# Kernel tuning notes

Measured on AMD Instinct MI355X. Metric: run time of the kernel, lower is better.

The kernel has to match this reference:

```python
import jax, jax.numpy as jnp
import numpy as np

C, H, W = 128, 128, 128
N_LINES = 8192
N_POINTS = 32
POOL = 4
DIM_FC = 1024


def setup_inputs() -> dict:
    key = jax.random.key(0)
    ks = jax.random.split(key, 8)
    feats = jax.random.normal(ks[0], (C, H, W), dtype=jnp.float32)
    # line endpoints (x1,y1,x2,y2) in feature-map pixel coords
    lines = jax.random.uniform(ks[1], (N_LINES, 4), dtype=jnp.float32) * (H - 1)
    d_in = C * (N_POINTS // POOL)  # 1024
    W1 = jax.random.normal(ks[2], (DIM_FC, d_in), dtype=jnp.float32) * 0.02
    b1 = jax.random.normal(ks[3], (DIM_FC,), dtype=jnp.float32) * 0.02
    W2 = jax.random.normal(ks[4], (DIM_FC, DIM_FC), dtype=jnp.float32) * 0.02
    b2 = jax.random.normal(ks[5], (DIM_FC,), dtype=jnp.float32) * 0.02
    W3 = jax.random.normal(ks[6], (4, DIM_FC), dtype=jnp.float32) * 0.02
    b3 = jax.random.normal(ks[7], (4,), dtype=jnp.float32) * 0.02
    return {
        "features_per_image": feats,
        "lines_per_im": lines,
        "W1": W1, "b1": b1, "W2": W2, "b2": b2, "W3": W3, "b3": b3,
        "n_points": N_POINTS,
        "pool_stride": POOL,
    }


def _extract_pt_feats(features, lines, n_points):
    # features: [C, H, W]; lines: [N, 4]
    c, h, w = features.shape
    tspan = jnp.linspace(0.0, 1.0, n_points).astype(features.dtype)  # [P]
    U, V = lines[:, :2], lines[:, 2:]
    # [N, 2, P] -> interpolate endpoints, shift by 0.5 (torch pixel-center convention)
    pts = U[:, :, None] * tspan + V[:, :, None] * (1.0 - tspan) - 0.5
    pts = pts.transpose(0, 2, 1).reshape(-1, 2)  # [N*P, 2]
    px, py = pts[:, 0], pts[:, 1]
    # NOTE: faithful to torch source: px indexes the h-axis but is clamped with w-1,
    # py indexes the w-axis but is clamped with h-1 (harmless here since H == W).
    px0 = jnp.clip(jnp.floor(px), 0.0, w - 1)
    py0 = jnp.clip(jnp.floor(py), 0.0, h - 1)
    px1 = jnp.clip(px0 + 1.0, 0.0, w - 1)
    py1 = jnp.clip(py0 + 1.0, 0.0, h - 1)
    px0i, py0i = px0.astype(jnp.int32), py0.astype(jnp.int32)
    px1i, py1i = px1.astype(jnp.int32), py1.astype(jnp.int32)
    # four irregular gathers + bilinear weights, fused expression. each term: [C, N*P]
    xp = (features[:, px0i, py0i] * ((py1 - py) * (px1 - px))
          + features[:, px0i, py1i] * ((py - py0) * (px1 - px))
          + features[:, px1i, py0i] * ((py1 - py) * (px - px0))
          + features[:, px1i, py1i] * ((py - py0) * (px - px0)))
    return xp.reshape(c, -1, n_points).transpose(1, 0, 2)  # [N, C, P]


def reference(features_per_image, lines_per_im, W1, b1, W2, b2, W3, b3,
              n_points, pool_stride):
    xp = _extract_pt_feats(features_per_image, lines_per_im, n_points)  # [N, C, P]
    n, c, p = xp.shape
    # MaxPool1d(kernel=stride=pool_stride)
    pooled = xp.reshape(n, c, p // pool_stride, pool_stride).max(axis=-1)
    flat = pooled.reshape(n, -1)  # [N, C*(P//s)]
    h1 = jax.nn.relu(flat @ W1.T + b1)
    h2 = jax.nn.relu(h1 @ W2.T + b2)
    return h2 @ W3.T + b3  # [N, 4]
```

## Files before the change

### kernel.cpp

```cpp
#include <hip/hip_runtime.h>
#include <hip/hip_bf16.h>
#include <cstdint>

typedef __attribute__((ext_vector_type(4))) float f32x4;
typedef __attribute__((ext_vector_type(8))) short short8;

#define DEVI __device__ __forceinline__

DEVI uint16_t f2bf(float v) {
    union { float f; uint32_t u; } c; c.f = v;
    uint32_t u = c.u + 0x7FFFu + ((c.u >> 16) & 1u);
    return (uint16_t)(u >> 16);
}
DEVI float bflo(uint32_t u) { union { uint32_t u; float f; } c; c.u = u << 16; return c.f; }
DEVI float bfhi(uint32_t u) { union { uint32_t u; float f; } c; c.u = u & 0xFFFF0000u; return c.f; }

DEVI void async16(const uint16_t* g, uint16_t* l) {
    __builtin_amdgcn_global_load_lds((const __attribute__((address_space(1))) void*)g,
                                     (__attribute__((address_space(3))) void*)l, 16, 0, 0);
}

__global__ __launch_bounds__(256) void prep_feat(const float* __restrict__ f,
                                                 uint16_t* __restrict__ featT) {
    __shared__ uint16_t s[128 * 130];
    const int x = blockIdx.x;
    const float* fx = f + x * 128;
    for (int i = threadIdx.x; i < 16384; i += 256) {
        int c = i >> 7, y = i & 127;
        s[y * 130 + c] = f2bf(fx[c * 16384 + y]);
    }
    __syncthreads();
    uint16_t* o = featT + x * 16384;
    for (int i = threadIdx.x; i < 16384; i += 256) {
        int y = i >> 7, c = i & 127;
        o[i] = s[y * 130 + c];
    }
}

__global__ __launch_bounds__(256) void cvt_w(const float* __restrict__ W1, uint16_t* __restrict__ W1b,
                                             const float* __restrict__ W2, uint16_t* __restrict__ W2b) {
    int i = blockIdx.x * 256 + threadIdx.x;
    float4 a = ((const float4*)W1)[i];
    float4 b = ((const float4*)W2)[i];
    ushort4 pa = { f2bf(a.x), f2bf(a.y), f2bf(a.z), f2bf(a.w) };
    ushort4 pb = { f2bf(b.x), f2bf(b.y), f2bf(b.z), f2bf(b.w) };
    ((ushort4*)W1b)[i] = pa;
    ((ushort4*)W2b)[i] = pb;
}

__global__ __launch_bounds__(256) void extract_k(const float4* __restrict__ lines,
                                                 const uint16_t* __restrict__ featT,
                                                 uint16_t* __restrict__ flat) {
    const int n = blockIdx.x;
    const int tid = threadIdx.x;
    const int lane = tid & 63, wave = tid >> 6;
    const float4 ln = lines[n];
    __shared__ uint16_t ps[1024];
    const uint16_t* fb = featT + lane * 2;

    for (int g2 = 0; g2 < 2; ++g2) {
        const int g = wave * 2 + g2;
        float m0 = -1e30f, m1 = -1e30f;
#pragma unroll
        for (int pp = 0; pp < 4; ++pp) {
            const float t = (float)(g * 4 + pp) * (1.0f / 31.0f);
            const float x = ln.x * t + ln.z * (1.0f - t) - 0.5f;
            const float y = ln.y * t + ln.w * (1.0f - t) - 0.5f;
            const float x0f = fminf(fmaxf(floorf(x), 0.0f), 127.0f);
            const float y0f = fminf(fmaxf(floorf(y), 0.0f), 127.0f);
            const float x1f = fminf(x0f + 1.0f, 127.0f);
            const float y1f = fminf(y0f + 1.0f, 127.0f);
            const int x0 = (int)x0f, x1 = (int)x1f, y0 = (int)y0f, y1 = (int)y1f;
            const float wx1 = x - x0f, wx0 = x1f - x;
            const float wy1 = y - y0f, wy0 = y1f - y;
            const uint32_t u00 = *(const uint32_t*)(fb + ((x0 * 128 + y0) << 7));
            const uint32_t u01 = *(const uint32_t*)(fb + ((x0 * 128 + y1) << 7));
            const uint32_t u10 = *(const uint32_t*)(fb + ((x1 * 128 + y0) << 7));
            const uint32_t u11 = *(const uint32_t*)(fb + ((x1 * 128 + y1) << 7));
            const float w00 = wy0 * wx0, w01 = wy1 * wx0, w10 = wy0 * wx1, w11 = wy1 * wx1;
            const float a = bflo(u00) * w00 + bflo(u01) * w01 + bflo(u10) * w10 + bflo(u11) * w11;
            const float b = bfhi(u00) * w00 + bfhi(u01) * w01 + bfhi(u10) * w10 + bfhi(u11) * w11;
            m0 = fmaxf(m0, a);
            m1 = fmaxf(m1, b);
        }
        ps[lane * 16 + g]     = f2bf(m0);
        ps[lane * 16 + 8 + g] = f2bf(m1);
    }
    __syncthreads();
    *(uint2*)(flat + (size_t)n * 1024 + tid * 4) = ((const uint2*)ps)[tid];
}

template <int RELU>
__global__ __launch_bounds__(256) void gemm_bt(const uint16_t* __restrict__ A,
                                               const uint16_t* __restrict__ B,
                                               const float* __restrict__ bias,
                                               uint16_t* __restrict__ Co,
                                               int M, int N, int K) {
    __shared__ uint16_t As[128 * 32];
    __shared__ uint16_t Bs[128 * 32];
    const int tid = threadIdx.x;
    const int lane = tid & 63, wave = tid >> 6;
    const int nbm = M >> 7;
    const int bm = blockIdx.x % nbm;
    const int bn = blockIdx.x / nbm;
    const int wr = wave >> 1, wc = wave & 1;
    const int l15 = lane & 15, l16 = lane >> 4;

    f32x4 acc[4][4] = {};

    const uint16_t* Ag = A + (size_t)(bm * 128) * K;
    const uint16_t* Bg = B + (size_t)(bn * 128) * K;

    for (int kt = 0; kt < K; kt += 32) {
        if (kt) __syncthreads();
#pragma unroll
        for (int i = 0; i < 2; ++i) {
            const int c = i * 256 + tid;
            const int row = c >> 2, off = (c & 3) * 8;
            async16(Ag + (size_t)row * K + kt + off, &As[c * 8]);
            async16(Bg + (size_t)row * K + kt + off, &Bs[c * 8]);
        }
        __syncthreads();
        short8 a[4], b[4];
#pragma unroll
        for (int fm = 0; fm < 4; ++fm)
            a[fm] = *(const short8*)&As[(wr * 64 + fm * 16 + l15) * 32 + l16 * 8];
#pragma unroll
        for (int fn = 0; fn < 4; ++fn)
            b[fn] = *(const short8*)&Bs[(wc * 64 + fn * 16 + l15) * 32 + l16 * 8];
#pragma unroll
        for (int fm = 0; fm < 4; ++fm)
#pragma unroll
            for (int fn = 0; fn < 4; ++fn)
                acc[fm][fn] = __builtin_amdgcn_mfma_f32_16x16x32_bf16(a[fm], b[fn], acc[fm][fn], 0, 0, 0);
    }

#pragma unroll
    for (int fm = 0; fm < 4; ++fm) {
        const int row = bm * 128 + wr * 64 + fm * 16 + l16 * 4;
#pragma unroll
        for (int fn = 0; fn < 4; ++fn) {
            const int col = bn * 128 + wc * 64 + fn * 16 + l15;
            const float bv = bias[col];
#pragma unroll
            for (int r = 0; r < 4; ++r) {
                float v = acc[fm][fn][r] + bv;
                if (RELU) v = fmaxf(v, 0.0f);
                Co[(size_t)(row + r) * N + col] = f2bf(v);
            }
        }
    }
}

__global__ __launch_bounds__(256) void gemm3_k(const uint16_t* __restrict__ h2,
                                               const float* __restrict__ W3,
                                               const float* __restrict__ b3,
                                               float* __restrict__ out) {
    const int wave = threadIdx.x >> 6, lane = threadIdx.x & 63;
    const int m = blockIdx.x * 4 + wave;
    const uint4* hr = (const uint4*)(h2 + (size_t)m * 1024 + lane * 16);
    const uint4 u0 = hr[0], u1 = hr[1];
    float h[16];
    h[0] = bflo(u0.x); h[1] = bfhi(u0.x); h[2] = bflo(u0.y); h[3] = bfhi(u0.y);
    h[4] = bflo(u0.z); h[5] = bfhi(u0.z); h[6] = bflo(u0.w); h[7] = bfhi(u0.w);
    h[8]  = bflo(u1.x); h[9]  = bfhi(u1.x); h[10] = bflo(u1.y); h[11] = bfhi(u1.y);
    h[12] = bflo(u1.z); h[13] = bfhi(u1.z); h[14] = bflo(u1.w); h[15] = bfhi(u1.w);
    float acc[4];
#pragma unroll
    for (int j = 0; j < 4; ++j) {
        const float4* wr = (const float4*)(W3 + j * 1024 + lane * 16);
        const float4 w0 = wr[0], w1 = wr[1], w2 = wr[2], w3 = wr[3];
        float s;
        s  = h[0] * w0.x;  s += h[1] * w0.y;  s += h[2] * w0.z;  s += h[3] * w0.w;
        s += h[4] * w1.x;  s += h[5] * w1.y;  s += h[6] * w1.z;  s += h[7] * w1.w;
        s += h[8] * w2.x;  s += h[9] * w2.y;  s += h[10] * w2.z; s += h[11] * w2.w;
        s += h[12] * w3.x; s += h[13] * w3.y; s += h[14] * w3.z; s += h[15] * w3.w;
        acc[j] = s;
    }
#pragma unroll
    for (int off = 32; off >= 1; off >>= 1) {
#pragma unroll
        for (int j = 0; j < 4; ++j) acc[j] += __shfl_xor(acc[j], off);
    }
    if (lane == 0) {
        float4 o = { acc[0] + b3[0], acc[1] + b3[1], acc[2] + b3[2], acc[3] + b3[3] };
        *(float4*)(out + (size_t)m * 4) = o;
    }
}

extern "C" void kernel_launch(void* const* d_in, const int* in_sizes, int n_in,
                              void* d_out, int out_size, void* d_ws, size_t ws_size,
                              hipStream_t stream) {
    const float* feats = (const float*)d_in[0];
    const float* lines = (const float*)d_in[1];
    const float* W1 = (const float*)d_in[2];
    const float* b1 = (const float*)d_in[3];
    const float* W2 = (const float*)d_in[4];
    const float* b2 = (const float*)d_in[5];
    const float* W3 = (const float*)d_in[6];
    const float* b3 = (const float*)d_in[7];
    float* out = (float*)d_out;

    char* ws = (char*)d_ws;
    uint16_t* featT = (uint16_t*)(ws);
    uint16_t* W1b   = (uint16_t*)(ws + (4u << 20));
    uint16_t* W2b   = (uint16_t*)(ws + (6u << 20));
    uint16_t* flat  = (uint16_t*)(ws + (8u << 20));
    uint16_t* h1    = (uint16_t*)(ws + (24u << 20));

    prep_feat<<<128, 256, 0, stream>>>(feats, featT);
    cvt_w<<<1024, 256, 0, stream>>>(W1, W1b, W2, W2b);
    extract_k<<<8192, 256, 0, stream>>>((const float4*)lines, featT, flat);
    gemm_bt<1><<<512, 256, 0, stream>>>(flat, W1b, b1, h1, 8192, 1024, 1024);
    gemm_bt<1><<<512, 256, 0, stream>>>(h1, W2b, b2, flat, 8192, 1024, 1024);
    gemm3_k<<<2048, 256, 0, stream>>>(flat, W3, b3, out);
}
```

Before: 98.32 us.

## Fuse final linear layer into second GEMM epilogue and widen K tile with swizzle

The third linear layer (1024->4) is folded into the second GEMM's epilogue. Each block applies ReLU to its tile of h2, multiplies by W3, reduces across lanes with shuffles, and atomically adds partial sums into an output that a new kernel pre-fills with b3. This removes the h2 round trip through memory and one kernel launch. The GEMM K tile grows from 32 to 64 with an XOR-swizzled LDS layout to cut bank conflicts and halve the barrier count, and the feature-transpose and weight-conversion prep kernels are merged into one launch. In exchange, fp32 atomics make the summation order nondeterministic.

```diff
diff --git a/kernel.cpp b/kernel.cpp
--- a/kernel.cpp
+++ b/kernel.cpp
@@ -20,32 +20,38 @@
                                      (__attribute__((address_space(3))) void*)l, 16, 0, 0);
 }
 
-__global__ __launch_bounds__(256) void prep_feat(const float* __restrict__ f,
-                                                 uint16_t* __restrict__ featT) {
-    __shared__ uint16_t s[128 * 130];
-    const int x = blockIdx.x;
-    const float* fx = f + x * 128;
-    for (int i = threadIdx.x; i < 16384; i += 256) {
-        int c = i >> 7, y = i & 127;
-        s[y * 130 + c] = f2bf(fx[c * 16384 + y]);
-    }
-    __syncthreads();
-    uint16_t* o = featT + x * 16384;
-    for (int i = threadIdx.x; i < 16384; i += 256) {
-        int y = i >> 7, c = i & 127;
-        o[i] = s[y * 130 + c];
-    }
-}
-
-__global__ __launch_bounds__(256) void cvt_w(const float* __restrict__ W1, uint16_t* __restrict__ W1b,
-                                             const float* __restrict__ W2, uint16_t* __restrict__ W2b) {
-    int i = blockIdx.x * 256 + threadIdx.x;
-    float4 a = ((const float4*)W1)[i];
-    float4 b = ((const float4*)W2)[i];
-    ushort4 pa = { f2bf(a.x), f2bf(a.y), f2bf(a.z), f2bf(a.w) };
-    ushort4 pb = { f2bf(b.x), f2bf(b.y), f2bf(b.z), f2bf(b.w) };
-    ((ushort4*)W1b)[i] = pa;
-    ((ushort4*)W2b)[i] = pb;
+__global__ __launch_bounds__(256) void init_out(float* __restrict__ out, const float* __restrict__ b3) {
+    const int i = blockIdx.x * 256 + threadIdx.x;
+    float4 b = { b3[0], b3[1], b3[2], b3[3] };
+    ((float4*)out)[i] = b;
+}
+
+__global__ __launch_bounds__(256) void prep_all(const float* __restrict__ f, uint16_t* __restrict__ featT,
+                                                const float* __restrict__ W1, uint16_t* __restrict__ W1b,
+                                                const float* __restrict__ W2, uint16_t* __restrict__ W2b) {
+    if (blockIdx.x < 128) {
+        __shared__ uint16_t s[128 * 130];
+        const int x = blockIdx.x;
+        const float* fx = f + x * 128;
+        for (int i = threadIdx.x; i < 16384; i += 256) {
+            int c = i >> 7, y = i & 127;
+            s[y * 130 + c] = f2bf(fx[c * 16384 + y]);
+        }
+        __syncthreads();
+        uint16_t* o = featT + x * 16384;
+        for (int i = threadIdx.x; i < 16384; i += 256) {
+            int y = i >> 7, c = i & 127;
+            o[i] = s[y * 130 + c];
+        }
+    } else {
+        const int i = (blockIdx.x - 128) * 256 + threadIdx.x;
+        float4 a = ((const float4*)W1)[i];
+        float4 b = ((const float4*)W2)[i];
+        ushort4 pa = { f2bf(a.x), f2bf(a.y), f2bf(a.z), f2bf(a.w) };
+        ushort4 pb = { f2bf(b.x), f2bf(b.y), f2bf(b.z), f2bf(b.w) };
+        ((ushort4*)W1b)[i] = pa;
+        ((ushort4*)W2b)[i] = pb;
+    }
 }
 
 __global__ __launch_bounds__(256) void extract_k(const float4* __restrict__ lines,
@@ -90,14 +96,16 @@
     *(uint2*)(flat + (size_t)n * 1024 + tid * 4) = ((const uint2*)ps)[tid];
 }
 
-template <int RELU>
+template <int FUSE3>
 __global__ __launch_bounds__(256) void gemm_bt(const uint16_t* __restrict__ A,
                                                const uint16_t* __restrict__ B,
                                                const float* __restrict__ bias,
                                                uint16_t* __restrict__ Co,
+                                               const float* __restrict__ W3,
+                                               float* __restrict__ out3,
                                                int M, int N, int K) {
-    __shared__ uint16_t As[128 * 32];
-    __shared__ uint16_t Bs[128 * 32];
+    __shared__ uint16_t As[128 * 64];
+    __shared__ uint16_t Bs[128 * 64];
     const int tid = threadIdx.x;
     const int lane = tid & 63, wave = tid >> 6;
     const int nbm = M >> 7;
@@ -111,80 +119,92 @@
     const uint16_t* Ag = A + (size_t)(bm * 128) * K;
     const uint16_t* Bg = B + (size_t)(bn * 128) * K;
 
-    for (int kt = 0; kt < K; kt += 32) {
+    for (int kt = 0; kt < K; kt += 64) {
         if (kt) __syncthreads();
 #pragma unroll
-        for (int i = 0; i < 2; ++i) {
+        for (int i = 0; i < 4; ++i) {
             const int c = i * 256 + tid;
-            const int row = c >> 2, off = (c & 3) * 8;
-            async16(Ag + (size_t)row * K + kt + off, &As[c * 8]);
-            async16(Bg + (size_t)row * K + kt + off, &Bs[c * 8]);
+            const int row = c >> 3, slot = c & 7;
+            const int s2 = slot ^ (row & 7);
+            async16(Ag + (size_t)row * K + kt + s2 * 8, &As[c * 8]);
+            async16(Bg + (size_t)row * K + kt + s2 * 8, &Bs[c * 8]);
         }
         __syncthreads();
-        short8 a[4], b[4];
-#pragma unroll
-        for (int fm = 0; fm < 4; ++fm)
-            a[fm] = *(const short8*)&As[(wr * 64 + fm * 16 + l15) * 32 + l16 * 8];
-#pragma unroll
-        for (int fn = 0; fn < 4; ++fn)
-            b[fn] = *(const short8*)&Bs[(wc * 64 + fn * 16 + l15) * 32 + l16 * 8];
-#pragma unroll
-        for (int fm = 0; fm < 4; ++fm)
-#pragma unroll
-            for (int fn = 0; fn < 4; ++fn)
-                acc[fm][fn] = __builtin_amdgcn_mfma_f32_16x16x32_bf16(a[fm], b[fn], acc[fm][fn], 0, 0, 0);
-    }
-
-#pragma unroll
-    for (int fm = 0; fm < 4; ++fm) {
-        const int row = bm * 128 + wr * 64 + fm * 16 + l16 * 4;
+        short8 a[4][2], b[4][2];
+#pragma unroll
+        for (int fm = 0; fm < 4; ++fm) {
+            const int r = wr * 64 + fm * 16 + l15;
+#pragma unroll
+            for (int kk = 0; kk < 2; ++kk) {
+                const int s2 = (kk * 4 + l16) ^ (r & 7);
+                a[fm][kk] = *(const short8*)&As[r * 64 + s2 * 8];
+            }
+        }
+#pragma unroll
+        for (int fn = 0; fn < 4; ++fn) {
+            const int r = wc * 64 + fn * 16 + l15;
+#pragma unroll
+            for (int kk = 0; kk < 2; ++kk) {
+                const int s2 = (kk * 4 + l16) ^ (r & 7);
+                b[fn][kk] = *(const short8*)&Bs[r * 64 + s2 * 8];
+            }
+        }
+#pragma unroll
+        for (int kk = 0; kk < 2; ++kk)
+#pragma unroll
+            for (int fm = 0; fm < 4; ++fm)
+#pragma unroll
+                for (int fn = 0; fn < 4; ++fn)
+                    acc[fm][fn] = __builtin_amdgcn_mfma_f32_16x16x32_bf16(a[fm][kk], b[fn][kk], acc[fm][fn], 0, 0, 0);
+    }
+
+    if (!FUSE3) {
+#pragma unroll
+        for (int fm = 0; fm < 4; ++fm) {
+            const int row = bm * 128 + wr * 64 + fm * 16 + l16 * 4;
+#pragma unroll
+            for (int fn = 0; fn < 4; ++fn) {
+                const int col = bn * 128 + wc * 64 + fn * 16 + l15;
+                const float bv = bias[col];
+#pragma unroll
+                for (int r = 0; r < 4; ++r) {
+                    float v = fmaxf(acc[fm][fn][r] + bv, 0.0f);
+                    Co[(size_t)(row + r) * N + col] = f2bf(v);
+                }
+            }
+        }
+    } else {
+        float bv[4], w3v[4][4];
 #pragma unroll
         for (int fn = 0; fn < 4; ++fn) {
             const int col = bn * 128 + wc * 64 + fn * 16 + l15;
-            const float bv = bias[col];
+            bv[fn] = bias[col];
+#pragma unroll
+            for (int j = 0; j < 4; ++j) w3v[j][fn] = W3[j * N + col];
+        }
+#pragma unroll
+        for (int fm = 0; fm < 4; ++fm) {
+            const int row = bm * 128 + wr * 64 + fm * 16 + l16 * 4;
 #pragma unroll
             for (int r = 0; r < 4; ++r) {
-                float v = acc[fm][fn][r] + bv;
-                if (RELU) v = fmaxf(v, 0.0f);
-                Co[(size_t)(row + r) * N + col] = f2bf(v);
-            }
-        }
-    }
-}
-
-__global__ __launch_bounds__(256) void gemm3_k(const uint16_t* __restrict__ h2,
-                                               const float* __restrict__ W3,
-                                               const float* __restrict__ b3,
-                                               float* __restrict__ out) {
-    const int wave = threadIdx.x >> 6, lane = threadIdx.x & 63;
-    const int m = blockIdx.x * 4 + wave;
-    const uint4* hr = (const uint4*)(h2 + (size_t)m * 1024 + lane * 16);
-    const uint4 u0 = hr[0], u1 = hr[1];
-    float h[16];
-    h[0] = bflo(u0.x); h[1] = bfhi(u0.x); h[2] = bflo(u0.y); h[3] = bfhi(u0.y);
-    h[4] = bflo(u0.z); h[5] = bfhi(u0.z); h[6] = bflo(u0.w); h[7] = bfhi(u0.w);
-    h[8]  = bflo(u1.x); h[9]  = bfhi(u1.x); h[10] = bflo(u1.y); h[11] = bfhi(u1.y);
-    h[12] = bflo(u1.z); h[13] = bfhi(u1.z); h[14] = bflo(u1.w); h[15] = bfhi(u1.w);
-    float acc[4];
-#pragma unroll
-    for (int j = 0; j < 4; ++j) {
-        const float4* wr = (const float4*)(W3 + j * 1024 + lane * 16);
-        const float4 w0 = wr[0], w1 = wr[1], w2 = wr[2], w3 = wr[3];
-        float s;
-        s  = h[0] * w0.x;  s += h[1] * w0.y;  s += h[2] * w0.z;  s += h[3] * w0.w;
-        s += h[4] * w1.x;  s += h[5] * w1.y;  s += h[6] * w1.z;  s += h[7] * w1.w;
-        s += h[8] * w2.x;  s += h[9] * w2.y;  s += h[10] * w2.z; s += h[11] * w2.w;
-        s += h[12] * w3.x; s += h[13] * w3.y; s += h[14] * w3.z; s += h[15] * w3.w;
-        acc[j] = s;
-    }
-#pragma unroll
-    for (int off = 32; off >= 1; off >>= 1) {
-#pragma unroll
-        for (int j = 0; j < 4; ++j) acc[j] += __shfl_xor(acc[j], off);
-    }
-    if (lane == 0) {
-        float4 o = { acc[0] + b3[0], acc[1] + b3[1], acc[2] + b3[2], acc[3] + b3[3] };
-        *(float4*)(out + (size_t)m * 4) = o;
+                float p[4] = { 0.0f, 0.0f, 0.0f, 0.0f };
+#pragma unroll
+                for (int fn = 0; fn < 4; ++fn) {
+                    const float hv = fmaxf(acc[fm][fn][r] + bv[fn], 0.0f);
+#pragma unroll
+                    for (int j = 0; j < 4; ++j) p[j] += hv * w3v[j][fn];
+                }
+#pragma unroll
+                for (int off = 1; off <= 8; off <<= 1)
+#pragma unroll
+                    for (int j = 0; j < 4; ++j) p[j] += __shfl_xor(p[j], off);
+                if (l15 == 0) {
+                    float* o = out3 + (size_t)(row + r) * 4;
+#pragma unroll
+                    for (int j = 0; j < 4; ++j) atomicAdd(o + j, p[j]);
+                }
+            }
+        }
     }
 }
 
@@ -208,10 +228,9 @@
     uint16_t* flat  = (uint16_t*)(ws + (8u << 20));
     uint16_t* h1    = (uint16_t*)(ws + (24u << 20));
 
-    prep_feat<<<128, 256, 0, stream>>>(feats, featT);
-    cvt_w<<<1024, 256, 0, stream>>>(W1, W1b, W2, W2b);
+    init_out<<<32, 256, 0, stream>>>(out, b3);
+    prep_all<<<1152, 256, 0, stream>>>(feats, featT, W1, W1b, W2, W2b);
     extract_k<<<8192, 256, 0, stream>>>((const float4*)lines, featT, flat);
-    gemm_bt<1><<<512, 256, 0, stream>>>(flat, W1b, b1, h1, 8192, 1024, 1024);
-    gemm_bt<1><<<512, 256, 0, stream>>>(h1, W2b, b2, flat, 8192, 1024, 1024);
-    gemm3_k<<<2048, 256, 0, stream>>>(flat, W3, b3, out);
-}
+    gemm_bt<0><<<512, 256, 0, stream>>>(flat, W1b, b1, h1, nullptr, nullptr, 8192, 1024, 1024);
+    gemm_bt<1><<<512, 256, 0, stream>>>(h1, W2b, b2, nullptr, W3, out, 8192, 1024, 1024);
+}
```

After: 108.3 us. 10.1% more time.
